# Kernel tuning notes

Hardware: AMD Instinct MI355X
Metric: run time of the kernel (lower is better)

## Reference

```python
import jax, jax.numpy as jnp
import numpy as np

B, N, DIM = 4, 2048, 512
HEADS, DIM_HEAD = 8, 64
INNER = HEADS * DIM_HEAD  # == DIM, so to_out is Identity
LN_EPS = 1e-5
MASK_FILL = 1e-8  # faithful to torch.where(mask, attn, 1e-08)


def setup_inputs() -> dict:
    key = jax.random.key(0)
    k1, k2 = jax.random.split(key)
    x = jax.random.normal(k1, (B, N, DIM), dtype=jnp.float32)
    gamma = jnp.ones((DIM,), dtype=jnp.float32)
    beta = jnp.zeros((DIM,), dtype=jnp.float32)
    w_qkv = jax.random.normal(k2, (3 * INNER, DIM), dtype=jnp.float32) * (DIM ** -0.5)
    mask = jnp.tril(jnp.ones((N, N), dtype=bool))  # causal boolean mask, asserted 2-D in source
    return {"x": x, "gamma": gamma, "beta": beta, "w_qkv": w_qkv, "mask": mask}


def reference(x, gamma, beta, w_qkv, mask):
    # LayerNorm over last dim
    mu = jnp.mean(x, axis=-1, keepdims=True)
    var = jnp.var(x, axis=-1, keepdims=True)
    h = (x - mu) * jax.lax.rsqrt(var + LN_EPS) * gamma + beta
    # qkv projection (no bias), chunk into q, k, v
    qkv = h @ w_qkv.T  # [B, N, 3*INNER]
    q, k, v = jnp.split(qkv, 3, axis=-1)

    def to_heads(t):  # b n (h d) -> b h n d
        return t.reshape(B, N, HEADS, DIM_HEAD).transpose(0, 2, 1, 3)

    q, k, v = to_heads(q), to_heads(k), to_heads(v)
    # NOTE: original forward does NOT apply self.scale
    attn = jnp.einsum('bhnd,bhmd->bhnm', q, k)
    attn = jnp.where(mask[None, None, :, :], attn, MASK_FILL)
    p = jax.nn.softmax(attn, axis=-1)
    out = jnp.einsum('bhnm,bhmd->bhnd', p, v)
    out = out.transpose(0, 2, 1, 3).reshape(B, N, INNER)  # b h n d -> b n (h d)
    return out  # to_out is Identity since INNER == DIM
```

## Files before the change

kernel.cpp:

```cpp
#include <hip/hip_runtime.h>
#include <hip/hip_bf16.h>
#include <math.h>

#define B_  4
#define N_  2048
#define DIM_ 512
#define HEADS_ 8
#define QKV_ 1536
#define MASK_C 1e-8f
#define M_FIX 12.0f
#define LOG2E 1.44269504f

typedef __bf16 bf16_t;
typedef bf16_t bf16x8 __attribute__((ext_vector_type(8)));
typedef float  f32x4  __attribute__((ext_vector_type(4)));

__device__ __forceinline__ bf16_t f2b(float x) { return (bf16_t)x; }
__device__ __forceinline__ float  b2f(bf16_t x) { return (float)x; }

__device__ __forceinline__ f32x4 mfma16(bf16x8 a, bf16x8 b, f32x4 c) {
    return __builtin_amdgcn_mfma_f32_16x16x32_bf16(a, b, c, 0, 0, 0);
}

__global__ __launch_bounds__(256) void ln_wsplit_kernel(const float* __restrict__ x,
                                                        const float* __restrict__ gamma,
                                                        const float* __restrict__ beta,
                                                        bf16_t* __restrict__ hh,
                                                        bf16_t* __restrict__ hl,
                                                        const float* __restrict__ wq,
                                                        bf16_t* __restrict__ wh,
                                                        bf16_t* __restrict__ wl) {
    int blk = blockIdx.x;
    int t = threadIdx.x;
    if (blk >= B_ * N_) {
        int i = ((blk - B_ * N_) * 256 + t) * 4;
        float4 v = *(const float4*)&wq[i];
        float vv[4] = {v.x, v.y, v.z, v.w};
        #pragma unroll
        for (int j = 0; j < 4; j++) {
            bf16_t hi = f2b(vv[j]);
            wh[i + j] = hi;
            wl[i + j] = f2b(vv[j] - b2f(hi));
        }
        return;
    }
    int row = blk;
    const float* xr = x + (size_t)row * DIM_;
    float2 xv = *(const float2*)&xr[2 * t];
    float e0 = xv.x, e1 = xv.y;
    float s  = e0 + e1;
    float sq = e0 * e0 + e1 * e1;
    for (int off = 32; off; off >>= 1) {
        s  += __shfl_xor(s, off);
        sq += __shfl_xor(sq, off);
    }
    __shared__ float red[8];
    int w = t >> 6;
    if ((t & 63) == 0) { red[w] = s; red[4 + w] = sq; }
    __syncthreads();
    float S  = red[0] + red[1] + red[2] + red[3];
    float SQ = red[4] + red[5] + red[6] + red[7];
    float mu = S * (1.0f / DIM_);
    float var = SQ * (1.0f / DIM_) - mu * mu;
    float rs = rsqrtf(var + 1e-5f);
    float2 gv = *(const float2*)&gamma[2 * t];
    float2 bv = *(const float2*)&beta[2 * t];
    float y0 = (e0 - mu) * rs * gv.x + bv.x;
    float y1 = (e1 - mu) * rs * gv.y + bv.y;
    size_t base = (size_t)row * DIM_ + 2 * t;
    bf16_t h0 = f2b(y0), h1 = f2b(y1);
    __align__(4) bf16_t hp[2] = {h0, h1};
    __align__(4) bf16_t lp[2] = {f2b(y0 - b2f(h0)), f2b(y1 - b2f(h1))};
    *(unsigned int*)&hh[base] = *(unsigned int*)hp;
    *(unsigned int*)&hl[base] = *(unsigned int*)lp;
}

__global__ __launch_bounds__(256, 3) void qkv_gemm(const bf16_t* __restrict__ hh,
                                                   const bf16_t* __restrict__ hl,
                                                   const bf16_t* __restrict__ wh,
                                                   const bf16_t* __restrict__ wl,
                                                   bf16_t* __restrict__ qh, bf16_t* __restrict__ ql,
                                                   bf16_t* __restrict__ kh, bf16_t* __restrict__ kl,
                                                   bf16_t* __restrict__ vth,
                                                   float* __restrict__ part) {
    __shared__ __align__(16) bf16_t smem[20480];
    bf16_t* Ah = smem;
    bf16_t* Al = smem + 5120;
    bf16_t* Bh = smem + 10240;
    bf16_t* Bl = smem + 15360;
    int bm = blockIdx.x & 63;
    int bn = blockIdx.x >> 6;
    int t = threadIdx.x;
    int w = t >> 6, lane = t & 63, quad = lane >> 4, l16 = lane & 15;

    f32x4 acc[2][8];
    #pragma unroll
    for (int i = 0; i < 2; i++)
        #pragma unroll
        for (int j = 0; j < 8; j++) acc[i][j] = (f32x4)(0.0f);

    int sr = t >> 1, skc = (t & 1) * 16;
    size_t gA = (size_t)(bm * 128 + sr) * 512 + skc;
    size_t gB = (size_t)(bn * 128 + sr) * 512 + skc;

    uint4 rAh0 = *(const uint4*)&hh[gA];
    uint4 rAh1 = *(const uint4*)&hh[gA + 8];
    uint4 rAl0 = *(const uint4*)&hl[gA];
    uint4 rAl1 = *(const uint4*)&hl[gA + 8];
    uint4 rBh0 = *(const uint4*)&wh[gB];
    uint4 rBh1 = *(const uint4*)&wh[gB + 8];
    uint4 rBl0 = *(const uint4*)&wl[gB];
    uint4 rBl1 = *(const uint4*)&wl[gB + 8];

    for (int k0 = 0; k0 < 512; k0 += 32) {
        __syncthreads();
        *(uint4*)&Ah[sr * 40 + skc]     = rAh0;
        *(uint4*)&Ah[sr * 40 + skc + 8] = rAh1;
        *(uint4*)&Al[sr * 40 + skc]     = rAl0;
        *(uint4*)&Al[sr * 40 + skc + 8] = rAl1;
        *(uint4*)&Bh[sr * 40 + skc]     = rBh0;
        *(uint4*)&Bh[sr * 40 + skc + 8] = rBh1;
        *(uint4*)&Bl[sr * 40 + skc]     = rBl0;
        *(uint4*)&Bl[sr * 40 + skc + 8] = rBl1;
        __syncthreads();

        if (k0 < 480) {
            int kn = k0 + 32;
            rAh0 = *(const uint4*)&hh[gA + kn];
            rAh1 = *(const uint4*)&hh[gA + kn + 8];
            rAl0 = *(const uint4*)&hl[gA + kn];
            rAl1 = *(const uint4*)&hl[gA + kn + 8];
            rBh0 = *(const uint4*)&wh[gB + kn];
            rBh1 = *(const uint4*)&wh[gB + kn + 8];
            rBl0 = *(const uint4*)&wl[gB + kn];
            rBl1 = *(const uint4*)&wl[gB + kn + 8];
        }

        bf16x8 aH[2], aL[2];
        #pragma unroll
        for (int mt = 0; mt < 2; mt++) {
            aH[mt] = *(const bf16x8*)&Ah[(w * 32 + mt * 16 + l16) * 40 + quad * 8];
            aL[mt] = *(const bf16x8*)&Al[(w * 32 + mt * 16 + l16) * 40 + quad * 8];
        }
        #pragma unroll
        for (int nt = 0; nt < 8; nt++) {
            bf16x8 bH = *(const bf16x8*)&Bh[(nt * 16 + l16) * 40 + quad * 8];
            bf16x8 bL = *(const bf16x8*)&Bl[(nt * 16 + l16) * 40 + quad * 8];
            #pragma unroll
            for (int mt = 0; mt < 2; mt++) {
                acc[mt][nt] = mfma16(aH[mt], bH, acc[mt][nt]);
                acc[mt][nt] = mfma16(aH[mt], bL, acc[mt][nt]);
                acc[mt][nt] = mfma16(aL[mt], bH, acc[mt][nt]);
            }
        }
    }

    if (bn < 8) {
        bf16_t* dsth = (bn < 4) ? qh : kh;
        bf16_t* dstl = (bn < 4) ? ql : kl;
        int ncol0 = (bn & 3) * 128 + (t & 15) * 8;
        int r0 = t >> 4;
        #pragma unroll
        for (int pass = 0; pass < 2; pass++) {
            __syncthreads();
            #pragma unroll
            for (int mt = 0; mt < 2; mt++)
                #pragma unroll
                for (int nt = 0; nt < 8; nt++)
                    #pragma unroll
                    for (int reg = 0; reg < 4; reg++) {
                        float v = acc[mt][nt][reg];
                        bf16_t hi = f2b(v);
                        bf16_t val = pass ? f2b(v - b2f(hi)) : hi;
                        smem[(w * 32 + mt * 16 + quad * 4 + reg) * 132 + nt * 16 + l16] = val;
                    }
            __syncthreads();
            bf16_t* dst = pass ? dstl : dsth;
            #pragma unroll
            for (int i = 0; i < 8; i++) {
                int row = r0 + i * 16;
                *(uint4*)&dst[(size_t)(bm * 128 + row) * 512 + ncol0] =
                    *(const uint4*)&smem[row * 132 + ((t & 15) * 8)];
            }
        }
    } else {
        int bb = bm >> 4, key0 = (bm & 15) * 128;
        int n = t & 127, mc = (t >> 7) * 64;
        int head = (bn - 8) * 2 + (n >> 6), dd = n & 63;
        size_t obase = ((size_t)((bb * 8 + head) * 64 + dd)) * 2048 + key0 + mc;
        float Ssum = 0.0f;
        #pragma unroll
        for (int pass = 0; pass < 2; pass++) {
            __syncthreads();
            #pragma unroll
            for (int mt = 0; mt < 2; mt++)
                #pragma unroll
                for (int nt = 0; nt < 8; nt++)
                    #pragma unroll
                    for (int reg = 0; reg < 4; reg++) {
                        float v = acc[mt][nt][reg];
                        bf16_t hi = f2b(v);
                        bf16_t val = pass ? f2b(v - b2f(hi)) : hi;
                        smem[(w * 32 + mt * 16 + quad * 4 + reg) * 132 + nt * 16 + l16] = val;
                    }
            __syncthreads();
            #pragma unroll
            for (int i = 0; i < 64; i += 8) {
                __align__(16) bf16_t v8[8];
                #pragma unroll
                for (int j = 0; j < 8; j++) {
                    v8[j] = smem[(mc + i + j) * 132 + n];
                    Ssum += b2f(v8[j]);
                }
                if (pass == 0)
                    *(uint4*)&vth[obase + i] = *(const uint4*)v8;
            }
        }
        int tt = (key0 >> 6) + (mc >> 6);
        part[((size_t)((bb * 8 + head) * 32 + tt)) * 64 + dd] = Ssum;
    }
}

__global__ __launch_bounds__(256, 2) void attn_kernel(const bf16_t* __restrict__ qh,
                                                      const bf16_t* __restrict__ ql,
                                                      const bf16_t* __restrict__ kh,
                                                      const bf16_t* __restrict__ kl,
                                                      const bf16_t* __restrict__ vth,
                                                      const float* __restrict__ part,
                                                      float* __restrict__ out) {
    __shared__ __align__(16) bf16_t smem[24576];
    __shared__ __align__(16) bf16_t Ps[4 * 16 * 76];
    __shared__ float sufl[4][64];
    char* lds = (char*)smem;

    int blk = blockIdx.x;
    int bh = blk & 31;
    int gi = blk >> 5;
    int g3 = gi & 7;
    int q4 = gi >> 3;
    int rt;
    if (q4 == 0)      rt = 31 - g3;
    else if (q4 == 1) rt = g3;
    else if (q4 == 2) rt = 23 - g3;
    else              rt = 8 + g3;
    int b = bh >> 3, head = bh & 7;
    int t = threadIdx.x;
    int w = t >> 6, lane = t & 63, quad = lane >> 4, l16 = lane & 15;

    {
        int d = t & 63, g = t >> 6;
        float s = 0.0f;
        for (int tt = rt + 1 + g; tt < 32; tt += 4)
            s += part[((size_t)bh * 32 + tt) * 64 + d];
        sufl[g][d] = s;
    }

    bf16x8 qAH[2], qAL[2];
    {
        int qrow = rt * 64 + w * 16 + l16;
        size_t g = ((size_t)(b * N_ + qrow)) * 512 + head * 64 + quad * 8;
        qAH[0] = *(const bf16x8*)&qh[g];
        qAH[1] = *(const bf16x8*)&qh[g + 32];
        qAL[0] = *(const bf16x8*)&ql[g];
        qAL[1] = *(const bf16x8*)&ql[g + 32];
    }
    bf16x8 ones;
    #pragma unroll
    for (int j = 0; j < 8; j++) ones[j] = f2b(1.0f);

    f32x4 O[4];
    #pragma unroll
    for (int nt = 0; nt < 4; nt++) O[nt] = (f32x4)(0.0f);
    f32x4 Lacc = (f32x4)(0.0f);
    const float mbias = M_FIX * LOG2E;

    int r = t >> 2, c16 = t & 3;
    int swz = (r & 7) << 4;
    int lk0 = r * 128 + ((c16 * 32)      ^ swz);
    int lk1 = r * 128 + ((c16 * 32 + 16) ^ swz);
    size_t gk = ((size_t)(b * N_ + r)) * 512 + head * 64 + c16 * 16;
    size_t gv = ((size_t)(bh * 64 + r)) * 2048 + c16 * 16;

    uint4 pKh0 = *(const uint4*)&kh[gk];
    uint4 pKh1 = *(const uint4*)&kh[gk + 8];
    uint4 pKl0 = *(const uint4*)&kl[gk];
    uint4 pKl1 = *(const uint4*)&kl[gk + 8];
    uint4 pVh0 = *(const uint4*)&vth[gv];
    uint4 pVh1 = *(const uint4*)&vth[gv + 8];
    *(uint4*)(lds + lk0)         = pKh0;
    *(uint4*)(lds + lk1)         = pKh1;
    *(uint4*)(lds + 8192 + lk0)  = pKl0;
    *(uint4*)(lds + 8192 + lk1)  = pKl1;
    *(uint4*)(lds + 16384 + lk0) = pVh0;
    *(uint4*)(lds + 16384 + lk1) = pVh1;
    __syncthreads();

    for (int jt = 0; jt <= rt; jt++) {
        char* cur = lds + (jt & 1) * 24576;
        char* nxt = lds + ((jt + 1) & 1) * 24576;

        if (jt < rt) {
            gk += (size_t)64 * 512;
            gv += 64;
            pKh0 = *(const uint4*)&kh[gk];
            pKh1 = *(const uint4*)&kh[gk + 8];
            pKl0 = *(const uint4*)&kl[gk];
            pKl1 = *(const uint4*)&kl[gk + 8];
            pVh0 = *(const uint4*)&vth[gv];
            pVh1 = *(const uint4*)&vth[gv + 8];
        }

        f32x4 S[4];
        #pragma unroll
        for (int nt = 0; nt < 4; nt++) S[nt] = (f32x4)(0.0f);
        __builtin_amdgcn_s_setprio(1);
        #pragma unroll
        for (int khf = 0; khf < 2; khf++) {
            #pragma unroll
            for (int nt = 0; nt < 4; nt++) {
                int row = nt * 16 + l16;
                int bc = (khf * 64 + quad * 16) ^ ((row & 7) << 4);
                bf16x8 bH = *(const bf16x8*)(cur + row * 128 + bc);
                bf16x8 bL = *(const bf16x8*)(cur + 8192 + row * 128 + bc);
                S[nt] = mfma16(qAH[khf], bH, S[nt]);
                S[nt] = mfma16(qAH[khf], bL, S[nt]);
                S[nt] = mfma16(qAL[khf], bH, S[nt]);
            }
        }
        __builtin_amdgcn_s_setprio(0);

        if (jt == rt) {
            int lrow = w * 16 + quad * 4;
            #pragma unroll
            for (int nt = 0; nt < 4; nt++)
                #pragma unroll
                for (int reg = 0; reg < 4; reg++)
                    if (nt * 16 + l16 > lrow + reg) S[nt][reg] = MASK_C;
        }

        #pragma unroll
        for (int nt = 0; nt < 4; nt++)
            #pragma unroll
            for (int reg = 0; reg < 4; reg++)
                Ps[(w * 16 + quad * 4 + reg) * 76 + nt * 16 + l16] =
                    f2b(exp2f(fmaf(S[nt][reg], LOG2E, -mbias)));

        bf16x8 pH[2];
        #pragma unroll
        for (int khf = 0; khf < 2; khf++)
            pH[khf] = *(const bf16x8*)&Ps[(w * 16 + l16) * 76 + khf * 32 + quad * 8];

        __builtin_amdgcn_s_setprio(1);
        #pragma unroll
        for (int khf = 0; khf < 2; khf++) Lacc = mfma16(pH[khf], ones, Lacc);

        #pragma unroll
        for (int khf = 0; khf < 2; khf++) {
            #pragma unroll
            for (int nt = 0; nt < 4; nt++) {
                int row = nt * 16 + l16;
                int bc = (khf * 64 + quad * 16) ^ ((row & 7) << 4);
                bf16x8 vB = *(const bf16x8*)(cur + 16384 + row * 128 + bc);
                O[nt] = mfma16(pH[khf], vB, O[nt]);
            }
        }
        __builtin_amdgcn_s_setprio(0);

        if (jt < rt) {
            *(uint4*)(nxt + lk0)         = pKh0;
            *(uint4*)(nxt + lk1)         = pKh1;
            *(uint4*)(nxt + 8192 + lk0)  = pKl0;
            *(uint4*)(nxt + 8192 + lk1)  = pKl1;
            *(uint4*)(nxt + 16384 + lk0) = pVh0;
            *(uint4*)(nxt + 16384 + lk1) = pVh1;
        }
        __syncthreads();
    }

    float L[4];
    #pragma unroll
    for (int reg = 0; reg < 4; reg++) L[reg] = Lacc[reg];
    int cnt = N_ - (rt + 1) * 64;
    if (cnt > 0) {
        float pc = expf(MASK_C - M_FIX);
        float sv[4];
        #pragma unroll
        for (int nt = 0; nt < 4; nt++) {
            int d = nt * 16 + l16;
            sv[nt] = sufl[0][d] + sufl[1][d] + sufl[2][d] + sufl[3][d];
        }
        #pragma unroll
        for (int reg = 0; reg < 4; reg++) {
            L[reg] += pc * (float)cnt;
            #pragma unroll
            for (int nt = 0; nt < 4; nt++) O[nt][reg] += pc * sv[nt];
        }
    }

    #pragma unroll
    for (int reg = 0; reg < 4; reg++) {
        float rl = 1.0f / L[reg];
        int row = rt * 64 + w * 16 + quad * 4 + reg;
        #pragma unroll
        for (int nt = 0; nt < 4; nt++)
            out[((size_t)(b * N_ + row)) * DIM_ + head * 64 + nt * 16 + l16] =
                O[nt][reg] * rl;
    }
}

extern "C" void kernel_launch(void* const* d_in, const int* in_sizes, int n_in,
                              void* d_out, int out_size, void* d_ws, size_t ws_size,
                              hipStream_t stream) {
    const float* x     = (const float*)d_in[0];
    const float* gamma = (const float*)d_in[1];
    const float* beta  = (const float*)d_in[2];
    const float* w_qkv = (const float*)d_in[3];
    float* out = (float*)d_out;

    const size_t HW = (size_t)8192 * 512;
    const size_t WN = (size_t)1536 * 512;
    bf16_t* hh  = (bf16_t*)d_ws;
    bf16_t* hl  = hh + HW;
    bf16_t* qh  = hl + HW;
    bf16_t* ql  = qh + HW;
    bf16_t* kh  = ql + HW;
    bf16_t* kl  = kh + HW;
    bf16_t* vth = kl + HW;
    bf16_t* vtl = vth + HW;
    bf16_t* wh  = vtl + HW;
    bf16_t* wl  = wh + WN;
    float*  part = (float*)(wl + WN);

    ln_wsplit_kernel<<<B_ * N_ + 768, 256, 0, stream>>>(x, gamma, beta, hh, hl,
                                                        w_qkv, wh, wl);
    qkv_gemm<<<768, 256, 0, stream>>>(hh, hl, wh, wl, qh, ql, kh, kl, vth, part);
    attn_kernel<<<1024, 256, 0, stream>>>(qh, ql, kh, kl, vth, part, out);
}
```

Baseline: 190.6 us.

## Use 128-row query tiles with 8 waves sharing each K/V tile

The attention kernel now runs 512 threads per block covering 128 query rows, so each staged 64-key K/V tile in LDS is reused by eight waves instead of four. Global-to-LDS staging is split across twice as many threads, and the causal masking and suffix handling are adjusted for the two diagonal tiles. The grid is halved to 512 blocks with a simpler scheduling order. This cuts K/V global traffic and staging per query row, at the cost of fewer blocks, coarser load balance, and wasted work on the extra diagonal tile.

```diff
diff --git a/kernel.cpp b/kernel.cpp
--- a/kernel.cpp
+++ b/kernel.cpp
@@ -221,7 +221,7 @@
     }
 }
 
-__global__ __launch_bounds__(256, 2) void attn_kernel(const bf16_t* __restrict__ qh,
+__global__ __launch_bounds__(512, 4) void attn_kernel(const bf16_t* __restrict__ qh,
                                                       const bf16_t* __restrict__ ql,
                                                       const bf16_t* __restrict__ kh,
                                                       const bf16_t* __restrict__ kl,
@@ -229,35 +229,30 @@
                                                       const float* __restrict__ part,
                                                       float* __restrict__ out) {
     __shared__ __align__(16) bf16_t smem[24576];
-    __shared__ __align__(16) bf16_t Ps[4 * 16 * 76];
-    __shared__ float sufl[4][64];
+    __shared__ __align__(16) bf16_t Ps[8 * 16 * 76];
+    __shared__ float sufl[8][64];
     char* lds = (char*)smem;
 
     int blk = blockIdx.x;
     int bh = blk & 31;
     int gi = blk >> 5;
-    int g3 = gi & 7;
-    int q4 = gi >> 3;
-    int rt;
-    if (q4 == 0)      rt = 31 - g3;
-    else if (q4 == 1) rt = g3;
-    else if (q4 == 2) rt = 23 - g3;
-    else              rt = 8 + g3;
+    int rt = (gi < 8) ? (15 - gi) : (gi - 8);
     int b = bh >> 3, head = bh & 7;
     int t = threadIdx.x;
     int w = t >> 6, lane = t & 63, quad = lane >> 4, l16 = lane & 15;
+    int jmax = 2 * rt + 1;
 
     {
         int d = t & 63, g = t >> 6;
         float s = 0.0f;
-        for (int tt = rt + 1 + g; tt < 32; tt += 4)
+        for (int tt = jmax + 1 + g; tt < 32; tt += 8)
             s += part[((size_t)bh * 32 + tt) * 64 + d];
         sufl[g][d] = s;
     }
 
     bf16x8 qAH[2], qAL[2];
     {
-        int qrow = rt * 64 + w * 16 + l16;
+        int qrow = rt * 128 + w * 16 + l16;
         size_t g = ((size_t)(b * N_ + qrow)) * 512 + head * 64 + quad * 8;
         qAH[0] = *(const bf16x8*)&qh[g];
         qAH[1] = *(const bf16x8*)&qh[g + 32];
@@ -274,40 +269,30 @@
     f32x4 Lacc = (f32x4)(0.0f);
     const float mbias = M_FIX * LOG2E;
 
-    int r = t >> 2, c16 = t & 3;
+    int r = t >> 3, c16 = t & 7;
     int swz = (r & 7) << 4;
-    int lk0 = r * 128 + ((c16 * 32)      ^ swz);
-    int lk1 = r * 128 + ((c16 * 32 + 16) ^ swz);
-    size_t gk = ((size_t)(b * N_ + r)) * 512 + head * 64 + c16 * 16;
-    size_t gv = ((size_t)(bh * 64 + r)) * 2048 + c16 * 16;
-
-    uint4 pKh0 = *(const uint4*)&kh[gk];
-    uint4 pKh1 = *(const uint4*)&kh[gk + 8];
-    uint4 pKl0 = *(const uint4*)&kl[gk];
-    uint4 pKl1 = *(const uint4*)&kl[gk + 8];
-    uint4 pVh0 = *(const uint4*)&vth[gv];
-    uint4 pVh1 = *(const uint4*)&vth[gv + 8];
-    *(uint4*)(lds + lk0)         = pKh0;
-    *(uint4*)(lds + lk1)         = pKh1;
-    *(uint4*)(lds + 8192 + lk0)  = pKl0;
-    *(uint4*)(lds + 8192 + lk1)  = pKl1;
-    *(uint4*)(lds + 16384 + lk0) = pVh0;
-    *(uint4*)(lds + 16384 + lk1) = pVh1;
+    int lk = r * 128 + ((c16 * 16) ^ swz);
+    size_t gk = ((size_t)(b * N_ + r)) * 512 + head * 64 + c16 * 8;
+    size_t gv = ((size_t)(bh * 64 + r)) * 2048 + c16 * 8;
+
+    uint4 pKh = *(const uint4*)&kh[gk];
+    uint4 pKl = *(const uint4*)&kl[gk];
+    uint4 pVh = *(const uint4*)&vth[gv];
+    *(uint4*)(lds + lk)         = pKh;
+    *(uint4*)(lds + 8192 + lk)  = pKl;
+    *(uint4*)(lds + 16384 + lk) = pVh;
     __syncthreads();
 
-    for (int jt = 0; jt <= rt; jt++) {
+    for (int jt = 0; jt <= jmax; jt++) {
         char* cur = lds + (jt & 1) * 24576;
         char* nxt = lds + ((jt + 1) & 1) * 24576;
 
-        if (jt < rt) {
+        if (jt < jmax) {
             gk += (size_t)64 * 512;
             gv += 64;
-            pKh0 = *(const uint4*)&kh[gk];
-            pKh1 = *(const uint4*)&kh[gk + 8];
-            pKl0 = *(const uint4*)&kl[gk];
-            pKl1 = *(const uint4*)&kl[gk + 8];
-            pVh0 = *(const uint4*)&vth[gv];
-            pVh1 = *(const uint4*)&vth[gv + 8];
+            pKh = *(const uint4*)&kh[gk];
+            pKl = *(const uint4*)&kl[gk];
+            pVh = *(const uint4*)&vth[gv];
         }
 
         f32x4 S[4];
@@ -329,13 +314,15 @@
         }
         __builtin_amdgcn_s_setprio(0);
 
-        if (jt == rt) {
-            int lrow = w * 16 + quad * 4;
-            #pragma unroll
-            for (int nt = 0; nt < 4; nt++)
+        if (jt >= 2 * rt) {
+            int lrow = rt * 128 + w * 16 + quad * 4;
+            #pragma unroll
+            for (int nt = 0; nt < 4; nt++) {
+                int col = jt * 64 + nt * 16 + l16;
                 #pragma unroll
                 for (int reg = 0; reg < 4; reg++)
-                    if (nt * 16 + l16 > lrow + reg) S[nt][reg] = MASK_C;
+                    if (col > lrow + reg) S[nt][reg] = MASK_C;
+            }
         }
 
         #pragma unroll
@@ -366,28 +353,27 @@
         }
         __builtin_amdgcn_s_setprio(0);
 
-        if (jt < rt) {
-            *(uint4*)(nxt + lk0)         = pKh0;
-            *(uint4*)(nxt + lk1)         = pKh1;
-            *(uint4*)(nxt + 8192 + lk0)  = pKl0;
-            *(uint4*)(nxt + 8192 + lk1)  = pKl1;
-            *(uint4*)(nxt + 16384 + lk0) = pVh0;
-            *(uint4*)(nxt + 16384 + lk1) = pVh1;
+        if (jt < jmax) {
+            *(uint4*)(nxt + lk)         = pKh;
+            *(uint4*)(nxt + 8192 + lk)  = pKl;
+            *(uint4*)(nxt + 16384 + lk) = pVh;
         }
         __syncthreads();
     }
 
+    int ts = 2 * rt + 2;
+    int cnt = N_ - ts * 64;
     float L[4];
     #pragma unroll
     for (int reg = 0; reg < 4; reg++) L[reg] = Lacc[reg];
-    int cnt = N_ - (rt + 1) * 64;
     if (cnt > 0) {
         float pc = expf(MASK_C - M_FIX);
         float sv[4];
         #pragma unroll
         for (int nt = 0; nt < 4; nt++) {
             int d = nt * 16 + l16;
-            sv[nt] = sufl[0][d] + sufl[1][d] + sufl[2][d] + sufl[3][d];
+            sv[nt] = sufl[0][d] + sufl[1][d] + sufl[2][d] + sufl[3][d] +
+                     sufl[4][d] + sufl[5][d] + sufl[6][d] + sufl[7][d];
         }
         #pragma unroll
         for (int reg = 0; reg < 4; reg++) {
@@ -400,7 +386,7 @@
     #pragma unroll
     for (int reg = 0; reg < 4; reg++) {
         float rl = 1.0f / L[reg];
-        int row = rt * 64 + w * 16 + quad * 4 + reg;
+        int row = rt * 128 + w * 16 + quad * 4 + reg;
         #pragma unroll
         for (int nt = 0; nt < 4; nt++)
             out[((size_t)(b * N_ + row)) * DIM_ + head * 64 + nt * 16 + l16] =
@@ -434,5 +420,5 @@
     ln_wsplit_kernel<<<B_ * N_ + 768, 256, 0, stream>>>(x, gamma, beta, hh, hl,
                                                         w_qkv, wh, wl);
     qkv_gemm<<<768, 256, 0, stream>>>(hh, hl, wh, wl, qh, ql, kh, kl, vth, part);
-    attn_kernel<<<1024, 256, 0, stream>>>(qh, ql, kh, kl, vth, part, out);
+    attn_kernel<<<512, 512, 0, stream>>>(qh, ql, kh, kl, vth, part, out);
 }
```

Measured after the change: 190.8 us. About the same (+0.1%).
